# Performance work log

Measured on AMD Instinct MI355X. Metric: run time of the kernel, lower is better.

Reference implementation:

```python
import jax, jax.numpy as jnp
import numpy as np

N = 50000   # nodes
E = 800000  # edges (avg degree 16)
IN = 128
H = 128
OUT = 16
BN_EPS = 1e-5


def _uniform(key, shape, fan_in):
    s = 1.0 / np.sqrt(fan_in)
    return jax.random.uniform(key, shape, jnp.float32, -s, s)


def setup_inputs() -> dict:
    key = jax.random.key(0)
    ks = jax.random.split(key, 12)
    x = jax.random.normal(ks[0], (N, IN), jnp.float32)
    edge_index = jax.random.randint(ks[1], (2, E), 0, N, dtype=jnp.int64)
    # SAGEConv layer 1: lin_l (with bias) on aggregated neighbors, lin_r (no bias) on root
    Wl1 = _uniform(ks[2], (H, IN), IN)
    bl1 = _uniform(ks[3], (H,), IN)
    Wr1 = _uniform(ks[4], (H, IN), IN)
    # SAGEConv layer 2
    Wl2 = _uniform(ks[5], (OUT, H), H)
    bl2 = _uniform(ks[6], (OUT,), H)
    Wr2 = _uniform(ks[7], (OUT, H), H)
    # BatchNorm1d(H) affine params
    gamma = jnp.ones((H,), jnp.float32)
    beta = jnp.zeros((H,), jnp.float32)
    # PReLU single shared slope
    a = jnp.array(0.25, jnp.float32)
    return {"x": x, "edge_index": edge_index, "Wl1": Wl1, "bl1": bl1, "Wr1": Wr1,
            "Wl2": Wl2, "bl2": bl2, "Wr2": Wr2, "gamma": gamma, "beta": beta, "a": a}


def sage_conv(x, src, dst, Wl, bl, Wr):
    # mean-aggregate source features at destination nodes
    msg = x[src]                                              # [E, F] gather
    summ = jax.ops.segment_sum(msg, dst, num_segments=N)      # [N, F] scatter-add
    cnt = jax.ops.segment_sum(jnp.ones((src.shape[0],), x.dtype), dst, num_segments=N)
    agg = summ / jnp.clip(cnt, 1.0)[:, None]
    return agg @ Wl.T + bl + x @ Wr.T


def reference(x, edge_index, Wl1, bl1, Wr1, Wl2, bl2, Wr2, gamma, beta, a):
    src, dst = edge_index[0], edge_index[1]
    # layer 1: SAGEConv -> BatchNorm (batch stats) -> PReLU -> residual
    h = sage_conv(x, src, dst, Wl1, bl1, Wr1)
    mean = h.mean(axis=0)
    var = h.var(axis=0)  # biased, as in torch BN training
    h = gamma * (h - mean) / jnp.sqrt(var + BN_EPS) + beta
    h = jnp.where(h >= 0, h, a * h)  # PReLU (shared slope)
    h = h + x  # residual (hidden == in)
    # layer 2 + log_softmax over classes
    out = sage_conv(h, src, dst, Wl2, bl2, Wr2)
    return jax.nn.log_softmax(out, axis=1)
```

## Files before the change

kernel.cpp:

```cpp
#include <hip/hip_runtime.h>

#define NNODES 50000
#define EEDGES 800000
#define FIN 128
#define FH 128
#define FOUT 16
#define BN_EPS 1e-5f
#define NBIN 391
#define CAP 4096
#define PCH 2048
#define NPB 391
#define NTILES 1563

typedef short bf16x8 __attribute__((ext_vector_type(8)));
typedef float f32x4 __attribute__((ext_vector_type(4)));

__device__ inline unsigned short tobf16(float f) {
    unsigned int u = __float_as_uint(f);
    u += 0x7fffu + ((u >> 16) & 1u);
    return (unsigned short)(u >> 16);
}
__device__ inline float frombf16(unsigned short h) {
    return __uint_as_float(((unsigned int)h) << 16);
}
__device__ inline unsigned packbf(float f0, float f1) {
    return (unsigned)tobf16(f0) | ((unsigned)tobf16(f1) << 16);
}
__device__ inline float lo16(unsigned u) { return __uint_as_float(u << 16); }
__device__ inline float hi16(unsigned u) { return __uint_as_float(u & 0xffff0000u); }

__global__ void pack_kernel(const float* __restrict__ x,
                            const float* __restrict__ Wl1, const float* __restrict__ Wr1,
                            const float* __restrict__ Wl2, const float* __restrict__ Wr2,
                            unsigned short* __restrict__ xb, unsigned short* __restrict__ wb) {
    int t = blockIdx.x * 256 + threadIdx.x;
    int base = t * 8;
    const float* srcp;
    unsigned short* dstp;
    int off;
    if (base < NNODES * FIN) {
        srcp = x; off = base; dstp = xb + base;
    } else {
        int w = base - NNODES * FIN;
        if (w >= 36864) return;
        dstp = wb + w;
        if (w < 16384)      { srcp = Wl1; off = w; }
        else if (w < 32768) { srcp = Wr1; off = w - 16384; }
        else if (w < 34816) { srcp = Wl2; off = w - 32768; }
        else                { srcp = Wr2; off = w - 34816; }
    }
    float4 f0 = *reinterpret_cast<const float4*>(srcp + off);
    float4 f1 = *reinterpret_cast<const float4*>(srcp + off + 4);
    uint4 r;
    r.x = packbf(f0.x, f0.y);
    r.y = packbf(f0.z, f0.w);
    r.z = packbf(f1.x, f1.y);
    r.w = packbf(f1.z, f1.w);
    *reinterpret_cast<uint4*>(dstp) = r;
}

__global__ void partition_kernel(const int* __restrict__ src, const int* __restrict__ dst,
                                 int* __restrict__ binFill, unsigned int* __restrict__ edgeBin) {
    __shared__ int hist[NBIN];
    __shared__ int runBase[NBIN];
    __shared__ int runFill[NBIN];
    int t = threadIdx.x;
    for (int i = t; i < NBIN; i += 256) { hist[i] = 0; runFill[i] = 0; }
    __syncthreads();
    int e0 = blockIdx.x * PCH;
    for (int i = 0; i < PCH / 256; ++i) {
        int e = e0 + i * 256 + t;
        if (e < EEDGES) atomicAdd(&hist[dst[e] >> 7], 1);
    }
    __syncthreads();
    for (int i = t; i < NBIN; i += 256) {
        int c = hist[i];
        if (c) runBase[i] = atomicAdd(&binFill[i], c);
    }
    __syncthreads();
    for (int i = 0; i < PCH / 256; ++i) {
        int e = e0 + i * 256 + t;
        if (e < EEDGES) {
            int d = dst[e];
            int b = d >> 7;
            int off = runBase[b] + atomicAdd(&runFill[b], 1);
            if (off < CAP)
                edgeBin[(size_t)b * CAP + off] = ((unsigned)(d & 127) << 17) | (unsigned)src[e];
        }
    }
}

__global__ void binscan_kernel(const unsigned int* __restrict__ edgeBin,
                               const int* __restrict__ binFill,
                               int* __restrict__ localPrefix) {
    __shared__ int cnt[128];
    __shared__ int sc[128];
    int b = blockIdx.x;
    int t = threadIdx.x;
    if (t < 128) cnt[t] = 0;
    __syncthreads();
    int n = binFill[b];
    for (int k = t; k < n; k += 256)
        atomicAdd(&cnt[edgeBin[(size_t)b * CAP + k] >> 17], 1);
    __syncthreads();
    if (t < 128) sc[t] = cnt[t];
    __syncthreads();
    for (int off = 1; off < 128; off <<= 1) {
        int v = (t < 128 && t >= off) ? sc[t - off] : 0;
        __syncthreads();
        if (t < 128) sc[t] += v;
        __syncthreads();
    }
    if (t < 128) localPrefix[b * 128 + t] = sc[t] - cnt[t];
}

__global__ void scanbins_kernel(const int* __restrict__ binFill, int* __restrict__ binOff) {
    __shared__ int sh[512];
    int t = threadIdx.x;
    int v = (t < NBIN) ? binFill[t] : 0;
    sh[t] = v;
    __syncthreads();
    for (int off = 1; off < 512; off <<= 1) {
        int u = (t >= off) ? sh[t - off] : 0;
        __syncthreads();
        sh[t] += u;
        __syncthreads();
    }
    if (t < NBIN) binOff[t] = sh[t] - v;
}

__global__ void local_bucket_kernel(const unsigned int* __restrict__ edgeBin,
                                    const int* __restrict__ binFill,
                                    const int* __restrict__ binOff,
                                    const int* __restrict__ localPrefix,
                                    int* __restrict__ srcSorted,
                                    int* __restrict__ rowstart) {
    __shared__ int wp[128];
    int b = blockIdx.x;
    int t = threadIdx.x;
    if (t < 128) {
        int node = b * 128 + t;
        int rs = binOff[b] + localPrefix[b * 128 + t];
        wp[t] = rs;
        if (node < NNODES) rowstart[node] = rs;
    }
    if (b == 0 && t == 128) rowstart[NNODES] = EEDGES;
    __syncthreads();
    int n = binFill[b];
    for (int k = t; k < n; k += 256) {
        unsigned c = edgeBin[(size_t)b * CAP + k];
        int p = atomicAdd(&wp[c >> 17], 1);
        srcSorted[p] = (int)(c & 0x1FFFF);
    }
}

__global__ void gather_bf16(const unsigned short* __restrict__ feat,
                            const int* __restrict__ rowstart,
                            const int* __restrict__ srcSorted,
                            unsigned short* __restrict__ aggout) {
    int tid = threadIdx.x;
    int i = blockIdx.x * 4 + (tid >> 6);
    int j = tid & 63;
    const unsigned int* fp = (const unsigned int*)feat;
    int k0 = rowstart[i], k1 = rowstart[i + 1];
    float a0 = 0.0f, a1 = 0.0f;
    int k = k0;
    for (; k + 4 <= k1; k += 4) {
        int s0 = srcSorted[k], s1 = srcSorted[k + 1], s2 = srcSorted[k + 2], s3 = srcSorted[k + 3];
        unsigned int u0 = fp[(size_t)s0 * 64 + j];
        unsigned int u1 = fp[(size_t)s1 * 64 + j];
        unsigned int u2 = fp[(size_t)s2 * 64 + j];
        unsigned int u3 = fp[(size_t)s3 * 64 + j];
        a0 += lo16(u0) + lo16(u1) + lo16(u2) + lo16(u3);
        a1 += hi16(u0) + hi16(u1) + hi16(u2) + hi16(u3);
    }
    for (; k < k1; ++k) {
        unsigned int u = fp[(size_t)srcSorted[k] * 64 + j];
        a0 += lo16(u);
        a1 += hi16(u);
    }
    float inv = 1.0f / (float)max(k1 - k0, 1);
    ((unsigned int*)aggout)[(size_t)i * 64 + j] = packbf(a0 * inv, a1 * inv);
}

__global__ void __launch_bounds__(256, 2)
lin1_persist(const unsigned short* __restrict__ aggb,
             const unsigned short* __restrict__ xb,
             const unsigned short* __restrict__ wl,
             const unsigned short* __restrict__ wr,
             const float* __restrict__ bias,
             unsigned short* __restrict__ hb,
             float* __restrict__ bnsum, float* __restrict__ bnsq) {
    __shared__ float bps[128];
    __shared__ float bpq[128];
    int tid = threadIdx.x;
    if (tid < 128) { bps[tid] = 0.0f; bpq[tid] = 0.0f; }
    __syncthreads();
    int wave = tid >> 6;
    int lane = tid & 63;
    int c = wave & 1;
    int rsub = wave >> 1;
    int lrow = lane & 15;
    int kg = lane >> 4;

    bf16x8 wlF[4][4], wrF[4][4];
    #pragma unroll
    for (int nf = 0; nf < 4; ++nf) {
        #pragma unroll
        for (int ks = 0; ks < 4; ++ks) {
            wlF[nf][ks] = *(const bf16x8*)(wl + (size_t)(c * 64 + nf * 16 + lrow) * 128 + ks * 32 + kg * 8);
            wrF[nf][ks] = *(const bf16x8*)(wr + (size_t)(c * 64 + nf * 16 + lrow) * 128 + ks * 32 + kg * 8);
        }
    }
    float bias_v[4];
    #pragma unroll
    for (int nf = 0; nf < 4; ++nf) bias_v[nf] = bias[c * 64 + nf * 16 + lrow];

    for (int tIt = blockIdx.x; tIt < NTILES; tIt += gridDim.x) {
        int rowA = tIt * 32 + rsub * 16 + lrow;
        int arow = min(rowA, NNODES - 1);
        bf16x8 aA[4], aX[4];
        #pragma unroll
        for (int ks = 0; ks < 4; ++ks) {
            aA[ks] = *(const bf16x8*)(aggb + (size_t)arow * 128 + ks * 32 + kg * 8);
            aX[ks] = *(const bf16x8*)(xb + (size_t)arow * 128 + ks * 32 + kg * 8);
        }
        f32x4 acc[4] = {};
        #pragma unroll
        for (int ks = 0; ks < 4; ++ks) {
            #pragma unroll
            for (int nf = 0; nf < 4; ++nf) {
                acc[nf] = __builtin_amdgcn_mfma_f32_16x16x32_bf16(aA[ks], wlF[nf][ks], acc[nf], 0, 0, 0);
                acc[nf] = __builtin_amdgcn_mfma_f32_16x16x32_bf16(aX[ks], wrF[nf][ks], acc[nf], 0, 0, 0);
            }
        }
        #pragma unroll
        for (int nf = 0; nf < 4; ++nf) {
            float s = 0.0f, q = 0.0f;
            #pragma unroll
            for (int rr = 0; rr < 4; ++rr) {
                int row = tIt * 32 + rsub * 16 + kg * 4 + rr;
                if (row < NNODES) {
                    unsigned short hv = tobf16(acc[nf][rr] + bias_v[nf]);
                    float vr = frombf16(hv);
                    hb[(size_t)row * 128 + c * 64 + nf * 16 + lrow] = hv;
                    s += vr; q += vr * vr;
                }
            }
            s += __shfl_xor(s, 16); s += __shfl_xor(s, 32);
            q += __shfl_xor(q, 16); q += __shfl_xor(q, 32);
            if (lane < 16) {
                atomicAdd(&bps[c * 64 + nf * 16 + lane], s);
                atomicAdd(&bpq[c * 64 + nf * 16 + lane], q);
            }
        }
    }
    __syncthreads();
    if (tid < 128) {
        atomicAdd(&bnsum[tid], bps[tid]);
        atomicAdd(&bnsq[tid], bpq[tid]);
    }
}

__global__ void bn_apply_kernel(unsigned short* __restrict__ hb,
                                const unsigned short* __restrict__ xb,
                                const float* __restrict__ gamma, const float* __restrict__ beta,
                                const float* __restrict__ aptr,
                                const float* __restrict__ bnsum, const float* __restrict__ bnsq) {
    int idx = blockIdx.x * 256 + threadIdx.x;
    if (idx >= NNODES * FH) return;
    int j = idx & 127;
    const float invN = 1.0f / (float)NNODES;
    float mean = bnsum[j] * invN;
    float var = bnsq[j] * invN - mean * mean;
    float istd = rsqrtf(var + BN_EPS);
    float v = frombf16(hb[idx]);
    v = gamma[j] * (v - mean) * istd + beta[j];
    float a = aptr[0];
    v = (v >= 0.0f) ? v : a * v;
    hb[idx] = tobf16(v + frombf16(xb[idx]));
}

__global__ void lin2a_kernel(const unsigned short* __restrict__ hb,
                             const unsigned short* __restrict__ wl,
                             unsigned short* __restrict__ y2) {
    int wave = threadIdx.x >> 6;
    int lane = threadIdx.x & 63;
    int row0 = blockIdx.x * 64 + wave * 16;
    int lrow = lane & 15;
    int kg = lane >> 4;
    int arow = min(row0 + lrow, NNODES - 1);
    f32x4 acc = {};
    #pragma unroll
    for (int ks = 0; ks < 4; ++ks) {
        bf16x8 a = *(const bf16x8*)(hb + (size_t)arow * 128 + ks * 32 + kg * 8);
        bf16x8 b = *(const bf16x8*)(wl + (size_t)lrow * 128 + ks * 32 + kg * 8);
        acc = __builtin_amdgcn_mfma_f32_16x16x32_bf16(a, b, acc, 0, 0, 0);
    }
    #pragma unroll
    for (int r = 0; r < 4; ++r) {
        int row = row0 + kg * 4 + r;
        if (row < NNODES)
            y2[(size_t)row * 16 + lrow] = tobf16(acc[r]);
    }
}

__global__ void gather16_kernel(const unsigned short* __restrict__ y2,
                                const int* __restrict__ rowstart,
                                const int* __restrict__ srcSorted,
                                unsigned short* __restrict__ agg2) {
    int tid = threadIdx.x;
    int i = blockIdx.x * 4 + (tid >> 6);
    int lane = tid & 63;
    int e = lane >> 3;
    int j = lane & 7;
    const unsigned int* yp = (const unsigned int*)y2;
    int k0 = rowstart[i], k1 = rowstart[i + 1];
    float a0 = 0.0f, a1 = 0.0f;
    for (int k = k0; k < k1; k += 8) {
        int kk = k + e;
        if (kk < k1) {
            unsigned u = yp[(size_t)srcSorted[kk] * 8 + j];
            a0 += lo16(u);
            a1 += hi16(u);
        }
    }
    a0 += __shfl_xor(a0, 8);  a1 += __shfl_xor(a1, 8);
    a0 += __shfl_xor(a0, 16); a1 += __shfl_xor(a1, 16);
    a0 += __shfl_xor(a0, 32); a1 += __shfl_xor(a1, 32);
    if (e == 0) {
        float inv = 1.0f / (float)max(k1 - k0, 1);
        ((unsigned int*)agg2)[(size_t)i * 8 + j] = packbf(a0 * inv, a1 * inv);
    }
}

__global__ void lin2b_kernel(const unsigned short* __restrict__ agg2,
                             const unsigned short* __restrict__ hb,
                             const unsigned short* __restrict__ wr,
                             const float* __restrict__ bias,
                             float* __restrict__ out) {
    int wave = threadIdx.x >> 6;
    int lane = threadIdx.x & 63;
    int row0 = blockIdx.x * 64 + wave * 16;
    int lrow = lane & 15;
    int kg = lane >> 4;
    int arow = min(row0 + lrow, NNODES - 1);
    f32x4 acc = {};
    #pragma unroll
    for (int ks = 0; ks < 4; ++ks) {
        bf16x8 a = *(const bf16x8*)(hb + (size_t)arow * 128 + ks * 32 + kg * 8);
        bf16x8 b = *(const bf16x8*)(wr + (size_t)lrow * 128 + ks * 32 + kg * 8);
        acc = __builtin_amdgcn_mfma_f32_16x16x32_bf16(a, b, acc, 0, 0, 0);
    }
    float bl = bias[lrow];
    #pragma unroll
    for (int r = 0; r < 4; ++r) {
        int row = row0 + kg * 4 + r;
        int rowc = min(row, NNODES - 1);
        float v = acc[r] + bl + frombf16(agg2[(size_t)rowc * 16 + lrow]);
        float m = v;
        for (int s = 1; s < 16; s <<= 1) m = fmaxf(m, __shfl_xor(m, s, 16));
        float ex = expf(v - m);
        float se = ex;
        for (int s = 1; s < 16; s <<= 1) se += __shfl_xor(se, s, 16);
        if (row < NNODES)
            out[(size_t)row * FOUT + lrow] = v - m - logf(se);
    }
}

extern "C" void kernel_launch(void* const* d_in, const int* in_sizes, int n_in,
                              void* d_out, int out_size, void* d_ws, size_t ws_size,
                              hipStream_t stream) {
    const float* x    = (const float*)d_in[0];
    const int*   ei   = (const int*)d_in[1];
    const int*   src  = ei;
    const int*   dst  = ei + EEDGES;
    const float* Wl1  = (const float*)d_in[2];
    const float* bl1  = (const float*)d_in[3];
    const float* Wr1  = (const float*)d_in[4];
    const float* Wl2  = (const float*)d_in[5];
    const float* bl2  = (const float*)d_in[6];
    const float* Wr2  = (const float*)d_in[7];
    const float* gamma= (const float*)d_in[8];
    const float* beta = (const float*)d_in[9];
    const float* a    = (const float*)d_in[10];
    float* out = (float*)d_out;

    char* W = (char*)d_ws;
    unsigned short* xb    = (unsigned short*)(W + 0);
    unsigned short* hb    = (unsigned short*)(W + 12800000);
    unsigned int*  edgeBin= (unsigned int*)(W + 25600000);
    unsigned short* aggb  = (unsigned short*)(W + 25600000);
    unsigned short* y2b   = (unsigned short*)(W + 25600000);
    unsigned short* agg2b = (unsigned short*)(W + 27200000);
    unsigned short* wb    = (unsigned short*)(W + 38400000);
    int* binFill  = (int*)(W + 38473728);
    float* bnsum  = (float*)(W + 38475292);
    float* bnsq   = (float*)(W + 38475804);
    int* binOff   = (int*)(W + 38476316);
    int* localPrefix = (int*)(W + 38477880);
    int* rowstart = (int*)(W + 38678072);
    int* srcSorted= (int*)(W + 38878076);

    unsigned short* wl1b = wb;
    unsigned short* wr1b = wb + 16384;
    unsigned short* wl2b = wb + 32768;
    unsigned short* wr2b = wb + 34816;

    hipMemsetAsync(binFill, 0, (size_t)2588, stream);

    pack_kernel<<<3143, 256, 0, stream>>>(x, Wl1, Wr1, Wl2, Wr2, xb, wb);
    partition_kernel<<<NPB, 256, 0, stream>>>(src, dst, binFill, edgeBin);
    binscan_kernel<<<NBIN, 256, 0, stream>>>(edgeBin, binFill, localPrefix);
    scanbins_kernel<<<1, 512, 0, stream>>>(binFill, binOff);
    local_bucket_kernel<<<NBIN, 256, 0, stream>>>(edgeBin, binFill, binOff, localPrefix,
                                                  srcSorted, rowstart);

    gather_bf16<<<NNODES / 4, 256, 0, stream>>>(xb, rowstart, srcSorted, aggb);
    lin1_persist<<<512, 256, 0, stream>>>(aggb, xb, wl1b, wr1b, bl1, hb, bnsum, bnsq);
    bn_apply_kernel<<<25000, 256, 0, stream>>>(hb, xb, gamma, beta, a, bnsum, bnsq);

    lin2a_kernel<<<782, 256, 0, stream>>>(hb, wl2b, y2b);
    gather16_kernel<<<NNODES / 4, 256, 0, stream>>>(y2b, rowstart, srcSorted, agg2b);
    lin2b_kernel<<<782, 256, 0, stream>>>(agg2b, hb, wr2b, bl2, out);
}
```

Measured before the change: 160.6 us.

## Merge pack/partition, binscan/scanbins, and BN-apply/lin2a kernels; unroll gather by 8

```diff
diff --git a/kernel.cpp b/kernel.cpp
--- a/kernel.cpp
+++ b/kernel.cpp
@@ -11,6 +11,7 @@
 #define PCH 2048
 #define NPB 391
 #define NTILES 1563
+#define PACKBLKS 3143
 
 typedef short bf16x8 __attribute__((ext_vector_type(8)));
 typedef float f32x4 __attribute__((ext_vector_type(4)));
@@ -29,104 +30,108 @@
 __device__ inline float lo16(unsigned u) { return __uint_as_float(u << 16); }
 __device__ inline float hi16(unsigned u) { return __uint_as_float(u & 0xffff0000u); }
 
-__global__ void pack_kernel(const float* __restrict__ x,
-                            const float* __restrict__ Wl1, const float* __restrict__ Wr1,
-                            const float* __restrict__ Wl2, const float* __restrict__ Wr2,
-                            unsigned short* __restrict__ xb, unsigned short* __restrict__ wb) {
-    int t = blockIdx.x * 256 + threadIdx.x;
-    int base = t * 8;
-    const float* srcp;
-    unsigned short* dstp;
-    int off;
-    if (base < NNODES * FIN) {
-        srcp = x; off = base; dstp = xb + base;
-    } else {
-        int w = base - NNODES * FIN;
-        if (w >= 36864) return;
-        dstp = wb + w;
-        if (w < 16384)      { srcp = Wl1; off = w; }
-        else if (w < 32768) { srcp = Wr1; off = w - 16384; }
-        else if (w < 34816) { srcp = Wl2; off = w - 32768; }
-        else                { srcp = Wr2; off = w - 34816; }
-    }
-    float4 f0 = *reinterpret_cast<const float4*>(srcp + off);
-    float4 f1 = *reinterpret_cast<const float4*>(srcp + off + 4);
-    uint4 r;
-    r.x = packbf(f0.x, f0.y);
-    r.y = packbf(f0.z, f0.w);
-    r.z = packbf(f1.x, f1.y);
-    r.w = packbf(f1.z, f1.w);
-    *reinterpret_cast<uint4*>(dstp) = r;
-}
-
-__global__ void partition_kernel(const int* __restrict__ src, const int* __restrict__ dst,
-                                 int* __restrict__ binFill, unsigned int* __restrict__ edgeBin) {
+__global__ void part_pack_kernel(const int* __restrict__ src, const int* __restrict__ dst,
+                                 int* __restrict__ binFill, unsigned int* __restrict__ edgeBin,
+                                 const float* __restrict__ x,
+                                 const float* __restrict__ Wl1, const float* __restrict__ Wr1,
+                                 const float* __restrict__ Wl2, const float* __restrict__ Wr2,
+                                 unsigned short* __restrict__ xb, unsigned short* __restrict__ wb) {
     __shared__ int hist[NBIN];
     __shared__ int runBase[NBIN];
     __shared__ int runFill[NBIN];
     int t = threadIdx.x;
-    for (int i = t; i < NBIN; i += 256) { hist[i] = 0; runFill[i] = 0; }
-    __syncthreads();
-    int e0 = blockIdx.x * PCH;
-    for (int i = 0; i < PCH / 256; ++i) {
-        int e = e0 + i * 256 + t;
-        if (e < EEDGES) atomicAdd(&hist[dst[e] >> 7], 1);
-    }
-    __syncthreads();
-    for (int i = t; i < NBIN; i += 256) {
-        int c = hist[i];
-        if (c) runBase[i] = atomicAdd(&binFill[i], c);
-    }
-    __syncthreads();
-    for (int i = 0; i < PCH / 256; ++i) {
-        int e = e0 + i * 256 + t;
-        if (e < EEDGES) {
-            int d = dst[e];
-            int b = d >> 7;
-            int off = runBase[b] + atomicAdd(&runFill[b], 1);
-            if (off < CAP)
-                edgeBin[(size_t)b * CAP + off] = ((unsigned)(d & 127) << 17) | (unsigned)src[e];
-        }
-    }
-}
-
-__global__ void binscan_kernel(const unsigned int* __restrict__ edgeBin,
-                               const int* __restrict__ binFill,
-                               int* __restrict__ localPrefix) {
-    __shared__ int cnt[128];
-    __shared__ int sc[128];
-    int b = blockIdx.x;
+    if (blockIdx.x < NPB) {
+        for (int i = t; i < NBIN; i += 256) { hist[i] = 0; runFill[i] = 0; }
+        __syncthreads();
+        int e0 = blockIdx.x * PCH;
+        for (int i = 0; i < PCH / 256; ++i) {
+            int e = e0 + i * 256 + t;
+            if (e < EEDGES) atomicAdd(&hist[dst[e] >> 7], 1);
+        }
+        __syncthreads();
+        for (int i = t; i < NBIN; i += 256) {
+            int c = hist[i];
+            if (c) runBase[i] = atomicAdd(&binFill[i], c);
+        }
+        __syncthreads();
+        for (int i = 0; i < PCH / 256; ++i) {
+            int e = e0 + i * 256 + t;
+            if (e < EEDGES) {
+                int d = dst[e];
+                int b = d >> 7;
+                int off = runBase[b] + atomicAdd(&runFill[b], 1);
+                if (off < CAP)
+                    edgeBin[(size_t)b * CAP + off] = ((unsigned)(d & 127) << 17) | (unsigned)src[e];
+            }
+        }
+    } else {
+        int tt = (blockIdx.x - NPB) * 256 + t;
+        int base = tt * 8;
+        const float* srcp;
+        unsigned short* dstp;
+        int off;
+        if (base < NNODES * FIN) {
+            srcp = x; off = base; dstp = xb + base;
+        } else {
+            int w = base - NNODES * FIN;
+            if (w >= 36864) return;
+            dstp = wb + w;
+            if (w < 16384)      { srcp = Wl1; off = w; }
+            else if (w < 32768) { srcp = Wr1; off = w - 16384; }
+            else if (w < 34816) { srcp = Wl2; off = w - 32768; }
+            else                { srcp = Wr2; off = w - 34816; }
+        }
+        float4 f0 = *reinterpret_cast<const float4*>(srcp + off);
+        float4 f1 = *reinterpret_cast<const float4*>(srcp + off + 4);
+        uint4 r;
+        r.x = packbf(f0.x, f0.y);
+        r.y = packbf(f0.z, f0.w);
+        r.z = packbf(f1.x, f1.y);
+        r.w = packbf(f1.z, f1.w);
+        *reinterpret_cast<uint4*>(dstp) = r;
+    }
+}
+
+__global__ void binscan_scan_kernel(const unsigned int* __restrict__ edgeBin,
+                                    const int* __restrict__ binFill,
+                                    int* __restrict__ localPrefix,
+                                    int* __restrict__ binOff) {
     int t = threadIdx.x;
-    if (t < 128) cnt[t] = 0;
-    __syncthreads();
-    int n = binFill[b];
-    for (int k = t; k < n; k += 256)
-        atomicAdd(&cnt[edgeBin[(size_t)b * CAP + k] >> 17], 1);
-    __syncthreads();
-    if (t < 128) sc[t] = cnt[t];
-    __syncthreads();
-    for (int off = 1; off < 128; off <<= 1) {
-        int v = (t < 128 && t >= off) ? sc[t - off] : 0;
-        __syncthreads();
-        if (t < 128) sc[t] += v;
-        __syncthreads();
-    }
-    if (t < 128) localPrefix[b * 128 + t] = sc[t] - cnt[t];
-}
-
-__global__ void scanbins_kernel(const int* __restrict__ binFill, int* __restrict__ binOff) {
-    __shared__ int sh[512];
-    int t = threadIdx.x;
-    int v = (t < NBIN) ? binFill[t] : 0;
-    sh[t] = v;
-    __syncthreads();
-    for (int off = 1; off < 512; off <<= 1) {
-        int u = (t >= off) ? sh[t - off] : 0;
-        __syncthreads();
-        sh[t] += u;
-        __syncthreads();
-    }
-    if (t < NBIN) binOff[t] = sh[t] - v;
+    if (blockIdx.x < NBIN) {
+        __shared__ int cnt[128];
+        __shared__ int sc[128];
+        int b = blockIdx.x;
+        if (t < 128) cnt[t] = 0;
+        __syncthreads();
+        int n = binFill[b];
+        for (int k = t; k < n; k += 256)
+            atomicAdd(&cnt[edgeBin[(size_t)b * CAP + k] >> 17], 1);
+        __syncthreads();
+        if (t < 128) sc[t] = cnt[t];
+        __syncthreads();
+        for (int off = 1; off < 128; off <<= 1) {
+            int v = (t < 128 && t >= off) ? sc[t - off] : 0;
+            __syncthreads();
+            if (t < 128) sc[t] += v;
+            __syncthreads();
+        }
+        if (t < 128) localPrefix[b * 128 + t] = sc[t] - cnt[t];
+    } else {
+        __shared__ int sh[512];
+        int v0 = (t < NBIN) ? binFill[t] : 0;
+        int v1 = (t + 256 < NBIN) ? binFill[t + 256] : 0;
+        sh[t] = v0; sh[t + 256] = v1;
+        __syncthreads();
+        for (int off = 1; off < 512; off <<= 1) {
+            int a0 = (t >= off) ? sh[t - off] : 0;
+            int a1 = (t + 256 >= off) ? sh[t + 256 - off] : 0;
+            __syncthreads();
+            sh[t] += a0; sh[t + 256] += a1;
+            __syncthreads();
+        }
+        if (t < NBIN) binOff[t] = sh[t] - v0;
+        if (t + 256 < NBIN) binOff[t + 256] = sh[t + 256] - v1;
+    }
 }
 
 __global__ void local_bucket_kernel(const unsigned int* __restrict__ edgeBin,
@@ -165,6 +170,20 @@
     int k0 = rowstart[i], k1 = rowstart[i + 1];
     float a0 = 0.0f, a1 = 0.0f;
     int k = k0;
+    for (; k + 8 <= k1; k += 8) {
+        int s0 = srcSorted[k],     s1 = srcSorted[k + 1], s2 = srcSorted[k + 2], s3 = srcSorted[k + 3];
+        int s4 = srcSorted[k + 4], s5 = srcSorted[k + 5], s6 = srcSorted[k + 6], s7 = srcSorted[k + 7];
+        unsigned int u0 = fp[(size_t)s0 * 64 + j];
+        unsigned int u1 = fp[(size_t)s1 * 64 + j];
+        unsigned int u2 = fp[(size_t)s2 * 64 + j];
+        unsigned int u3 = fp[(size_t)s3 * 64 + j];
+        unsigned int u4 = fp[(size_t)s4 * 64 + j];
+        unsigned int u5 = fp[(size_t)s5 * 64 + j];
+        unsigned int u6 = fp[(size_t)s6 * 64 + j];
+        unsigned int u7 = fp[(size_t)s7 * 64 + j];
+        a0 += lo16(u0) + lo16(u1) + lo16(u2) + lo16(u3) + lo16(u4) + lo16(u5) + lo16(u6) + lo16(u7);
+        a1 += hi16(u0) + hi16(u1) + hi16(u2) + hi16(u3) + hi16(u4) + hi16(u5) + hi16(u6) + hi16(u7);
+    }
     for (; k + 4 <= k1; k += 4) {
         int s0 = srcSorted[k], s1 = srcSorted[k + 1], s2 = srcSorted[k + 2], s3 = srcSorted[k + 3];
         unsigned int u0 = fp[(size_t)s0 * 64 + j];
@@ -262,40 +281,52 @@
     }
 }
 
-__global__ void bn_apply_kernel(unsigned short* __restrict__ hb,
+__global__ void bn_lin2a_kernel(unsigned short* __restrict__ hb,
                                 const unsigned short* __restrict__ xb,
                                 const float* __restrict__ gamma, const float* __restrict__ beta,
                                 const float* __restrict__ aptr,
-                                const float* __restrict__ bnsum, const float* __restrict__ bnsq) {
-    int idx = blockIdx.x * 256 + threadIdx.x;
-    if (idx >= NNODES * FH) return;
-    int j = idx & 127;
-    const float invN = 1.0f / (float)NNODES;
-    float mean = bnsum[j] * invN;
-    float var = bnsq[j] * invN - mean * mean;
-    float istd = rsqrtf(var + BN_EPS);
-    float v = frombf16(hb[idx]);
-    v = gamma[j] * (v - mean) * istd + beta[j];
-    float a = aptr[0];
-    v = (v >= 0.0f) ? v : a * v;
-    hb[idx] = tobf16(v + frombf16(xb[idx]));
-}
-
-__global__ void lin2a_kernel(const unsigned short* __restrict__ hb,
-                             const unsigned short* __restrict__ wl,
-                             unsigned short* __restrict__ y2) {
-    int wave = threadIdx.x >> 6;
-    int lane = threadIdx.x & 63;
+                                const float* __restrict__ bnsum, const float* __restrict__ bnsq,
+                                const unsigned short* __restrict__ wl,
+                                unsigned short* __restrict__ y2) {
+    __shared__ float scs[128];
+    __shared__ float shs[128];
+    int tid = threadIdx.x;
+    if (tid < 128) {
+        const float invN = 1.0f / (float)NNODES;
+        float mean = bnsum[tid] * invN;
+        float var = bnsq[tid] * invN - mean * mean;
+        float istd = rsqrtf(var + BN_EPS);
+        float sc = gamma[tid] * istd;
+        scs[tid] = sc;
+        shs[tid] = beta[tid] - mean * sc;
+    }
+    __syncthreads();
+    float aP = aptr[0];
+    int wave = tid >> 6;
+    int lane = tid & 63;
     int row0 = blockIdx.x * 64 + wave * 16;
     int lrow = lane & 15;
     int kg = lane >> 4;
-    int arow = min(row0 + lrow, NNODES - 1);
+    int rowA = row0 + lrow;
+    int arow = min(rowA, NNODES - 1);
     f32x4 acc = {};
     #pragma unroll
     for (int ks = 0; ks < 4; ++ks) {
-        bf16x8 a = *(const bf16x8*)(hb + (size_t)arow * 128 + ks * 32 + kg * 8);
+        bf16x8 hv = *(const bf16x8*)(hb + (size_t)arow * 128 + ks * 32 + kg * 8);
+        bf16x8 xv = *(const bf16x8*)(xb + (size_t)arow * 128 + ks * 32 + kg * 8);
+        bf16x8 nv;
+        #pragma unroll
+        for (int e = 0; e < 8; ++e) {
+            int f = ks * 32 + kg * 8 + e;
+            float v = frombf16((unsigned short)hv[e]) * scs[f] + shs[f];
+            v = (v >= 0.0f) ? v : aP * v;
+            v += frombf16((unsigned short)xv[e]);
+            nv[e] = (short)tobf16(v);
+        }
+        if (rowA < NNODES)
+            *(bf16x8*)(hb + (size_t)arow * 128 + ks * 32 + kg * 8) = nv;
         bf16x8 b = *(const bf16x8*)(wl + (size_t)lrow * 128 + ks * 32 + kg * 8);
-        acc = __builtin_amdgcn_mfma_f32_16x16x32_bf16(a, b, acc, 0, 0, 0);
+        acc = __builtin_amdgcn_mfma_f32_16x16x32_bf16(nv, b, acc, 0, 0, 0);
     }
     #pragma unroll
     for (int r = 0; r < 4; ++r) {
@@ -409,18 +440,17 @@
 
     hipMemsetAsync(binFill, 0, (size_t)2588, stream);
 
-    pack_kernel<<<3143, 256, 0, stream>>>(x, Wl1, Wr1, Wl2, Wr2, xb, wb);
-    partition_kernel<<<NPB, 256, 0, stream>>>(src, dst, binFill, edgeBin);
-    binscan_kernel<<<NBIN, 256, 0, stream>>>(edgeBin, binFill, localPrefix);
-    scanbins_kernel<<<1, 512, 0, stream>>>(binFill, binOff);
+    part_pack_kernel<<<NPB + PACKBLKS, 256, 0, stream>>>(src, dst, binFill, edgeBin,
+                                                         x, Wl1, Wr1, Wl2, Wr2, xb, wb);
+    binscan_scan_kernel<<<NBIN + 1, 256, 0, stream>>>(edgeBin, binFill, localPrefix, binOff);
     local_bucket_kernel<<<NBIN, 256, 0, stream>>>(edgeBin, binFill, binOff, localPrefix,
                                                   srcSorted, rowstart);
 
     gather_bf16<<<NNODES / 4, 256, 0, stream>>>(xb, rowstart, srcSorted, aggb);
     lin1_persist<<<512, 256, 0, stream>>>(aggb, xb, wl1b, wr1b, bl1, hb, bnsum, bnsq);
-    bn_apply_kernel<<<25000, 256, 0, stream>>>(hb, xb, gamma, beta, a, bnsum, bnsq);
-
-    lin2a_kernel<<<782, 256, 0, stream>>>(hb, wl2b, y2b);
+
+    bn_lin2a_kernel<<<782, 256, 0, stream>>>(hb, xb, gamma, beta, a, bnsum, bnsq, wl2b, y2b);
+
     gather16_kernel<<<NNODES / 4, 256, 0, stream>>>(y2b, rowstart, srcSorted, agg2b);
     lin2b_kernel<<<782, 256, 0, stream>>>(agg2b, hb, wr2b, bl2, out);
 }
```

New measurement: 141.9 us. -11.6%, faster.
